# Kernel tuning notes

Measured on AMD Instinct MI355X. Metric: run time of the kernel, lower is better.

## Reference

```python
import jax, jax.numpy as jnp
import numpy as np

B, S, D = 2, 1024, 4096
N_HEADS, KV_HEADS, HEAD_DIM = 32, 8, 128
EPS = 1e-6
ROPE_THETA = 1e6


def setup_inputs() -> dict:
    key = jax.random.key(0)
    ks = jax.random.split(key, 7)
    scale = 0.02
    x = jax.random.normal(ks[0], (B, S, D), dtype=jnp.float32)
    positions = jnp.broadcast_to(jnp.arange(S, dtype=jnp.int32)[None, :], (B, S))
    wq = jax.random.normal(ks[1], (D, N_HEADS, HEAD_DIM), dtype=jnp.float32) * scale
    wk = jax.random.normal(ks[2], (D, KV_HEADS, HEAD_DIM), dtype=jnp.float32) * scale
    wv = jax.random.normal(ks[3], (D, KV_HEADS, HEAD_DIM), dtype=jnp.float32) * scale
    wo = jax.random.normal(ks[4], (N_HEADS, HEAD_DIM, D), dtype=jnp.float32) * scale
    q_norm_w = 1.0 + jax.random.normal(ks[5], (HEAD_DIM,), dtype=jnp.float32) * 0.01
    k_norm_w = 1.0 + jax.random.normal(ks[6], (HEAD_DIM,), dtype=jnp.float32) * 0.01
    return {"x": x, "positions": positions, "wq": wq, "wk": wk, "wv": wv,
            "wo": wo, "q_norm_w": q_norm_w, "k_norm_w": k_norm_w}


def _rms_norm(t, w):
    # per-head RMSNorm over last (head_dim) axis
    var = jnp.mean(jnp.square(t), axis=-1, keepdims=True)
    return (t * jax.lax.rsqrt(var + EPS)) * w


def _rope(t, positions):
    # neox-style rotary embedding; t: [B, S, n, H], positions: [B, S]
    half = t.shape[-1] // 2
    inv_freq = 1.0 / (ROPE_THETA ** (jnp.arange(0, half, dtype=jnp.float32) / half))
    ang = positions.astype(jnp.float32)[..., None] * inv_freq  # [B, S, half]
    cos = jnp.cos(ang)[:, :, None, :]  # [B, S, 1, half]
    sin = jnp.sin(ang)[:, :, None, :]
    t1, t2 = t[..., :half], t[..., half:]
    return jnp.concatenate([t1 * cos - t2 * sin, t2 * cos + t1 * sin], axis=-1)


def reference(x, positions, wq, wk, wv, wo, q_norm_w, k_norm_w):
    # QKV projections (einsum layers: 'bsd,dnh->bsnh')
    q = jnp.einsum('bsd,dnh->bsnh', x, wq)  # [B, S, N, H]
    k = jnp.einsum('bsd,dkh->bskh', x, wk)  # [B, S, K, H]
    v = jnp.einsum('bsd,dkh->bskh', x, wv)
    # per-head QK RMSNorm, then RoPE
    q = _rope(_rms_norm(q, q_norm_w), positions)
    k = _rope(_rms_norm(k, k_norm_w), positions)
    # GQA: expand KV heads to query heads
    groups = N_HEADS // KV_HEADS
    k = jnp.repeat(k, groups, axis=2)  # [B, S, N, H]
    v = jnp.repeat(v, groups, axis=2)
    sm_scale = HEAD_DIM ** -0.5
    scores = jnp.einsum('bqnh,btnh->bnqt', q, k) * sm_scale  # [B, N, S, S]
    causal = jnp.tril(jnp.ones((S, S), dtype=bool))
    scores = jnp.where(causal[None, None], scores, jnp.finfo(scores.dtype).min)
    probs = jax.nn.softmax(scores, axis=-1)
    attn = jnp.einsum('bnqt,btnh->bqnh', probs, v)  # [B, S, N, H]
    out = jnp.einsum('bqnh,nhd->bqd', attn, wo)  # output projection
    return out
```

## Files before the change

kernel.cpp:

```cpp
#include <hip/hip_runtime.h>
#include <stdint.h>

#define S_LEN   1024
#define D_MODEL 4096
#define NHQ     32
#define NKV     8
#define HD      128
#define NTOK    2048
#define NQKV    6144
#define SM_SCALE 0.08838834764831843f

typedef __attribute__((ext_vector_type(8))) __bf16 bf16x8;
typedef __attribute__((ext_vector_type(4))) float f32x4;

__device__ __forceinline__ unsigned short f2bf(float f) {
  union { float f; unsigned u; } x; x.f = f;
  unsigned r = x.u + 0x7fffu + ((x.u >> 16) & 1u);
  return (unsigned short)(r >> 16);
}

__device__ __forceinline__ void gload_lds16(const void* g, void* l) {
  __builtin_amdgcn_global_load_lds((__attribute__((address_space(1))) void*)g,
                                   (__attribute__((address_space(3))) void*)l,
                                   16, 0, 0);
}

__global__ void k_f32_to_bf16(const float* __restrict__ in,
                              unsigned short* __restrict__ out, int n8) {
  int i = blockIdx.x * blockDim.x + threadIdx.x;
  if (i >= n8) return;
  const float4* p = (const float4*)(in + (size_t)i * 8);
  float4 v0 = p[0], v1 = p[1];
  uint4 o;
  o.x = f2bf(v0.x) | ((unsigned)f2bf(v0.y) << 16);
  o.y = f2bf(v0.z) | ((unsigned)f2bf(v0.w) << 16);
  o.z = f2bf(v1.x) | ((unsigned)f2bf(v1.y) << 16);
  o.w = f2bf(v1.z) | ((unsigned)f2bf(v1.w) << 16);
  *(uint4*)(out + (size_t)i * 8) = o;
}

__global__ void k_transpose(const float* __restrict__ in,
                            unsigned short* __restrict__ out, int R, int C) {
  __shared__ float t[32][33];
  int c = threadIdx.x & 31, r0 = threadIdx.x >> 5;
  int cb = blockIdx.x * 32, rb = blockIdx.y * 32;
#pragma unroll
  for (int i = 0; i < 4; ++i) {
    int r = r0 + i * 8;
    t[r][c] = in[(size_t)(rb + r) * C + cb + c];
  }
  __syncthreads();
#pragma unroll
  for (int i = 0; i < 4; ++i) {
    int r = r0 + i * 8;
    out[(size_t)(cb + r) * R + rb + c] = f2bf(t[c][r]);
  }
}

__global__ __launch_bounds__(256) void k_gemm(
    const unsigned short* __restrict__ A,
    const unsigned short* __restrict__ Bt,
    float* __restrict__ C, int M, int N, int K, int ldc) {
  __shared__ __align__(16) unsigned short aT[128 * 32];
  __shared__ __align__(16) unsigned short bT[128 * 32];
  int tid = threadIdx.x;
  int w = tid >> 6, l = tid & 63;
  int lr = l & 15, lg = l >> 4;
  int bm = blockIdx.y * 128, bn = blockIdx.x * 128;
  int wr = (w >> 1) * 64, wc = (w & 1) * 64;
  f32x4 acc[4][4] = {};
  for (int k0 = 0; k0 < K; k0 += 32) {
    __syncthreads();
#pragma unroll
    for (int it = 0; it < 2; ++it) {
      int eo = (tid + it * 256) * 8;
      int r = eo >> 5, c = eo & 31;
      gload_lds16(A + (size_t)(bm + r) * K + k0 + c, (unsigned short*)aT + eo);
      gload_lds16(Bt + (size_t)(bn + r) * K + k0 + c, (unsigned short*)bT + eo);
    }
    __syncthreads();
    bf16x8 af[4], bfr[4];
#pragma unroll
    for (int r = 0; r < 4; ++r)
      af[r] = *(const bf16x8*)&aT[(wr + r * 16 + lr) * 32 + lg * 8];
#pragma unroll
    for (int c = 0; c < 4; ++c)
      bfr[c] = *(const bf16x8*)&bT[(wc + c * 16 + lr) * 32 + lg * 8];
#pragma unroll
    for (int r = 0; r < 4; ++r)
#pragma unroll
      for (int c = 0; c < 4; ++c)
        acc[r][c] = __builtin_amdgcn_mfma_f32_16x16x32_bf16(af[r], bfr[c], acc[r][c], 0, 0, 0);
  }
#pragma unroll
  for (int r = 0; r < 4; ++r)
#pragma unroll
    for (int c = 0; c < 4; ++c)
#pragma unroll
      for (int j = 0; j < 4; ++j)
        C[(size_t)(bm + wr + r * 16 + lg * 4 + j) * ldc + bn + wc + c * 16 + lr] = acc[r][c][j];
}

__global__ void k_norm_rope(const float* __restrict__ qkv, const float* __restrict__ w,
                            const int* __restrict__ positions,
                            unsigned short* __restrict__ out, int nheads, int colbase,
                            float oscale) {
  int wid = blockIdx.x * 4 + (threadIdx.x >> 6);
  int lane = threadIdx.x & 63;
  int token = wid / nheads, head = wid - token * nheads;
  const float* src = qkv + (size_t)token * NQKV + colbase + head * HD;
  float e0 = src[lane], e1 = src[lane + 64];
  float ss = e0 * e0 + e1 * e1;
#pragma unroll
  for (int m = 1; m < 64; m <<= 1) ss += __shfl_xor(ss, m, 64);
  float rs = rsqrtf(ss * (1.0f / 128.0f) + 1e-6f);
  float n0 = e0 * rs * w[lane], n1 = e1 * rs * w[lane + 64];
  int pos = positions[token];
  float invf = exp2f((float)lane * (-19.931568569324174f / 64.0f));
  float ang = (float)pos * invf;
  float sv, cv;
  sincosf(ang, &sv, &cv);
  float o0 = (n0 * cv - n1 * sv) * oscale;
  float o1 = (n1 * cv + n0 * sv) * oscale;
  int b = token >> 10, s = token & 1023;
  size_t ob = ((size_t)(b * nheads + head) * S_LEN + s) * HD;
  out[ob + lane] = f2bf(o0);
  out[ob + 64 + lane] = f2bf(o1);
}

__global__ void k_v_transpose(const float* __restrict__ qkv, unsigned short* __restrict__ vt) {
  __shared__ float t[32][33];
  int slice = blockIdx.z;
  int b = slice >> 3, kh = slice & 7;
  const float* in = qkv + (size_t)(b * S_LEN) * NQKV + 5120 + kh * HD;
  unsigned short* out = vt + (size_t)slice * HD * S_LEN;
  int c = threadIdx.x & 31, r0 = threadIdx.x >> 5;
  int s0 = blockIdx.y * 32, d0 = blockIdx.x * 32;
#pragma unroll
  for (int i = 0; i < 4; ++i) {
    int r = r0 + i * 8;
    t[r][c] = in[(size_t)(s0 + r) * NQKV + d0 + c];
  }
  __syncthreads();
#pragma unroll
  for (int i = 0; i < 4; ++i) {
    int r = r0 + i * 8;
    out[(size_t)(d0 + r) * S_LEN + s0 + c] = f2bf(t[c][r]);
  }
}

__global__ __launch_bounds__(256) void k_attn(const unsigned short* __restrict__ qh,
                                              const unsigned short* __restrict__ kbuf,
                                              const unsigned short* __restrict__ vtbuf,
                                              unsigned short* __restrict__ attn_out) {
  __shared__ __align__(16) unsigned short k_lds[64 * 128];
  __shared__ __align__(16) unsigned short v_lds[128 * 64];
  __shared__ __align__(16) unsigned short p_lds[4][16 * 64];
  int b = blockIdx.z, h = blockIdx.y, bx = blockIdx.x;
  int khd = h >> 2;
  int tid = threadIdx.x, w = tid >> 6, l = tid & 63;
  int lr = l & 15, lg = l >> 4;
  const unsigned short* K = kbuf + (size_t)(b * NKV + khd) * S_LEN * HD;
  const unsigned short* VT = vtbuf + (size_t)(b * NKV + khd) * HD * S_LEN;
  char* klp = (char*)k_lds;
  char* vlp = (char*)v_lds;
  char* plp = (char*)p_lds[w];
  int swz = (lr & 7) << 4;

  for (int strip = 0; strip < 2; ++strip) {
    int qs = strip ? (15 - bx) : bx;
    int q0 = qs * 64;
    const unsigned short* Q = qh + ((size_t)(b * NHQ + h) * S_LEN + q0 + w * 16) * HD;
    bf16x8 qf[4];
#pragma unroll
    for (int kk = 0; kk < 4; ++kk)
      qf[kk] = *(const bf16x8*)&Q[(size_t)lr * HD + kk * 32 + lg * 8];

    f32x4 o[8] = {};
    float m_[4], l_[4];
#pragma unroll
    for (int j = 0; j < 4; ++j) { m_[j] = -1e30f; l_[j] = 0.0f; }

    int nt = qs + 1;
    for (int t = 0; t < nt; ++t) {
      int t0 = t * 64;
      __syncthreads();
#pragma unroll
      for (int it = 0; it < 4; ++it) {
        int db = (tid + it * 256) * 16;
        int kr = db >> 8, kc = db & 255;
        gload_lds16(K + (size_t)(t0 + kr) * HD + ((kc ^ ((kr & 7) << 4)) >> 1), klp + db);
        int vr = db >> 7, vc = db & 127;
        gload_lds16(VT + (size_t)vr * S_LEN + t0 + ((vc ^ ((vr & 7) << 4)) >> 1), vlp + db);
      }
      __syncthreads();

      f32x4 sc[4];
      __builtin_amdgcn_s_setprio(1);
#pragma unroll
      for (int ct = 0; ct < 4; ++ct) {
        f32x4 s = {};
        int row = ct * 16 + lr;
#pragma unroll
        for (int kk = 0; kk < 4; ++kk) {
          bf16x8 kf = *(const bf16x8*)(klp + row * 256 + ((kk * 64 + lg * 16) ^ swz));
          s = __builtin_amdgcn_mfma_f32_16x16x32_bf16(qf[kk], kf, s, 0, 0, 0);
        }
        sc[ct] = s;
      }
      __builtin_amdgcn_s_setprio(0);

      bool full = (t < qs);
      float alpha[4];
#pragma unroll
      for (int j = 0; j < 4; ++j) {
        if (!full) {
          int rg = q0 + w * 16 + lg * 4 + j;
#pragma unroll
          for (int ct = 0; ct < 4; ++ct)
            sc[ct][j] = (t0 + ct * 16 + lr <= rg) ? sc[ct][j] : -1e30f;
        }
        float mx = fmaxf(fmaxf(sc[0][j], sc[1][j]), fmaxf(sc[2][j], sc[3][j]));
#pragma unroll
        for (int msk = 1; msk < 16; msk <<= 1) mx = fmaxf(mx, __shfl_xor(mx, msk, 64));
        float mn = fmaxf(m_[j], mx);
        alpha[j] = __expf(m_[j] - mn);
        int q = lg * 4 + j;
        int psw = (q & 7) << 4;
        float ps = 0.0f;
#pragma unroll
        for (int ct = 0; ct < 4; ++ct) {
          float p = __expf(sc[ct][j] - mn);
          ps += p;
          *(unsigned short*)(plp + q * 128 + (((ct * 16 + lr) * 2) ^ psw)) = f2bf(p);
        }
#pragma unroll
        for (int msk = 1; msk < 16; msk <<= 1) ps += __shfl_xor(ps, msk, 64);
        l_[j] = l_[j] * alpha[j] + ps;
        m_[j] = mn;
      }
#pragma unroll
      for (int dc = 0; dc < 8; ++dc) {
        o[dc][0] *= alpha[0]; o[dc][1] *= alpha[1];
        o[dc][2] *= alpha[2]; o[dc][3] *= alpha[3];
      }
      asm volatile("s_waitcnt lgkmcnt(0)" ::: "memory");
      __builtin_amdgcn_s_setprio(1);
#pragma unroll
      for (int kt = 0; kt < 2; ++kt) {
        bf16x8 pa = *(const bf16x8*)(plp + lr * 128 + ((kt * 64 + lg * 16) ^ swz));
#pragma unroll
        for (int dc = 0; dc < 8; ++dc) {
          int vrow = dc * 16 + lr;
          bf16x8 vf = *(const bf16x8*)(vlp + vrow * 128 + ((kt * 64 + lg * 16) ^ swz));
          o[dc] = __builtin_amdgcn_mfma_f32_16x16x32_bf16(pa, vf, o[dc], 0, 0, 0);
        }
      }
      __builtin_amdgcn_s_setprio(0);
    }

#pragma unroll
    for (int j = 0; j < 4; ++j) {
      int rg = q0 + w * 16 + lg * 4 + j;
      size_t row = (size_t)(b * S_LEN + rg) * D_MODEL + h * HD;
      float inv = 1.0f / l_[j];
#pragma unroll
      for (int dc = 0; dc < 8; ++dc)
        attn_out[row + dc * 16 + lr] = f2bf(o[dc][j] * inv);
    }
  }
}

extern "C" void kernel_launch(void* const* d_in, const int* in_sizes, int n_in,
                              void* d_out, int out_size, void* d_ws, size_t ws_size,
                              hipStream_t stream) {
  const float* x        = (const float*)d_in[0];
  const int* positions  = (const int*)d_in[1];
  const float* wq       = (const float*)d_in[2];
  const float* wk       = (const float*)d_in[3];
  const float* wv       = (const float*)d_in[4];
  const float* wo       = (const float*)d_in[5];
  const float* qnw      = (const float*)d_in[6];
  const float* knw      = (const float*)d_in[7];
  float* out            = (float*)d_out;

  char* ws = (char*)d_ws;
  unsigned short* xb   = (unsigned short*)(ws);
  unsigned short* wB   = (unsigned short*)(ws + 16777216);
  unsigned short* woT  = (unsigned short*)(ws + 67108864);
  float*          qkv  = (float*)(ws + 100663296);
  unsigned short* qh   = wB;
  unsigned short* khb  = (unsigned short*)(ws + 33554432);
  unsigned short* vtb  = (unsigned short*)(ws + 37748736);
  unsigned short* attn = xb;

  dim3 tb(256);
  k_f32_to_bf16<<<4096, tb, 0, stream>>>(x, xb, 1048576);
  k_transpose<<<dim3(128, 128), tb, 0, stream>>>(wq, wB, 4096, 4096);
  k_transpose<<<dim3(32, 128), tb, 0, stream>>>(wk, wB + (size_t)4096 * 4096, 4096, 1024);
  k_transpose<<<dim3(32, 128), tb, 0, stream>>>(wv, wB + (size_t)5120 * 4096, 4096, 1024);
  k_transpose<<<dim3(128, 128), tb, 0, stream>>>(wo, woT, 4096, 4096);

  k_gemm<<<dim3(48, 16), tb, 0, stream>>>(xb, wB, qkv, 2048, 6144, 4096, 6144);

  k_norm_rope<<<16384, tb, 0, stream>>>(qkv, qnw, positions, qh, 32, 0, SM_SCALE);
  k_norm_rope<<<4096, tb, 0, stream>>>(qkv, knw, positions, khb, 8, 4096, 1.0f);
  k_v_transpose<<<dim3(4, 32, 16), tb, 0, stream>>>(qkv, vtb);

  k_attn<<<dim3(8, 32, 2), tb, 0, stream>>>(qh, khb, vtb, attn);

  k_gemm<<<dim3(32, 16), tb, 0, stream>>>(attn, woT, out, 2048, 4096, 4096, 4096);
}
```

Baseline: 402.7 us.

## Replace 128x128 GEMM with double-buffered 256x256 tile pipelined MFMA kernel

Replaces the simple single-buffered 128x128 GEMM with a 256x256-tile, 512-thread kernel using 128KB of dynamic LDS. It double-buffers K=64 stages, issuing async global-to-LDS loads interleaved with MFMA phases, and XOR-swizzles LDS rows to avoid bank conflicts. It also remaps workgroup IDs across XCDs, raises priority during MFMA issue, and uses manual waitcnt/barrier scheduling. Both the QKV and output projections use it. The 256x256 tiles give only 192 and 128 workgroups, which underfills a 256-CU GPU, and the hand-tuned waitcnts risk subtle races.

```diff
diff --git a/kernel.cpp b/kernel.cpp
--- a/kernel.cpp
+++ b/kernel.cpp
@@ -57,48 +57,93 @@
   }
 }
 
-__global__ __launch_bounds__(256) void k_gemm(
+
+#define STG(Gptr, rowbase, ksrc, half, bufi, matoff)                            \
+  { int kcl = (ksrc) < NT ? (ksrc) : NT - 1;                                    \
+    _Pragma("unroll")                                                           \
+    for (int i_ = 0; i_ < 2; ++i_) {                                            \
+      int lin = i_ * 512 + tid;                                                 \
+      int r_ = lin >> 2, slot = lin & 3;                                        \
+      int sw = slot ^ ((r_ >> 1) & 3);                                          \
+      gload_lds16(Gptr + (size_t)((rowbase) + r_) * K + kcl * 64 + (half) * 32 + sw * 8, \
+                  smem + (bufi) * 65536 + (matoff) + (half) * 16384 + lin * 16); \
+    } }
+
+#define PHASE(mh, kstep, STAGE_STMT, DO_VMCNT)                                  \
+  {                                                                             \
+    const char* Ab = smem + cur * 65536 + (kstep) * 16384;                      \
+    const char* Bb = smem + cur * 65536 + 32768 + (kstep) * 16384;              \
+    bf16x8 af[4], bfr[4];                                                       \
+    _Pragma("unroll")                                                           \
+    for (int mf = 0; mf < 4; ++mf) {                                            \
+      int row = wr * 128 + (mh) * 64 + mf * 16 + lr;                            \
+      af[mf] = *(const bf16x8*)(Ab + row * 64 + ((lg * 16) ^ (((row >> 1) & 3) << 4))); \
+    }                                                                           \
+    _Pragma("unroll")                                                           \
+    for (int nf = 0; nf < 4; ++nf) {                                            \
+      int row = wc * 64 + nf * 16 + lr;                                         \
+      bfr[nf] = *(const bf16x8*)(Bb + row * 64 + ((lg * 16) ^ (((row >> 1) & 3) << 4))); \
+    }                                                                           \
+    STAGE_STMT;                                                                 \
+    if (DO_VMCNT) asm volatile("s_waitcnt vmcnt(6)" ::: "memory");              \
+    __builtin_amdgcn_s_barrier();                                               \
+    asm volatile("s_waitcnt lgkmcnt(0)" ::: "memory");                          \
+    __builtin_amdgcn_sched_barrier(0);                                          \
+    __builtin_amdgcn_s_setprio(1);                                              \
+    _Pragma("unroll")                                                           \
+    for (int mf = 0; mf < 4; ++mf)                                              \
+      _Pragma("unroll")                                                         \
+      for (int nf = 0; nf < 4; ++nf)                                            \
+        acc[(mh) * 4 + mf][nf] =                                                \
+            __builtin_amdgcn_mfma_f32_16x16x32_bf16(af[mf], bfr[nf], acc[(mh) * 4 + mf][nf], 0, 0, 0); \
+    __builtin_amdgcn_s_setprio(0);                                              \
+    __builtin_amdgcn_s_barrier();                                               \
+  }
+
+__global__ __launch_bounds__(512, 2) void k_gemm256(
     const unsigned short* __restrict__ A,
     const unsigned short* __restrict__ Bt,
-    float* __restrict__ C, int M, int N, int K, int ldc) {
-  __shared__ __align__(16) unsigned short aT[128 * 32];
-  __shared__ __align__(16) unsigned short bT[128 * 32];
+    float* __restrict__ C, int M, int N, int K, int ldc, int nbx) {
+  extern __shared__ __align__(16) char smem[];
   int tid = threadIdx.x;
-  int w = tid >> 6, l = tid & 63;
+  int l = tid & 63;
+  int w = tid >> 6;
   int lr = l & 15, lg = l >> 4;
-  int bm = blockIdx.y * 128, bn = blockIdx.x * 128;
-  int wr = (w >> 1) * 64, wc = (w & 1) * 64;
-  f32x4 acc[4][4] = {};
-  for (int k0 = 0; k0 < K; k0 += 32) {
-    __syncthreads();
-#pragma unroll
-    for (int it = 0; it < 2; ++it) {
-      int eo = (tid + it * 256) * 8;
-      int r = eo >> 5, c = eo & 31;
-      gload_lds16(A + (size_t)(bm + r) * K + k0 + c, (unsigned short*)aT + eo);
-      gload_lds16(Bt + (size_t)(bn + r) * K + k0 + c, (unsigned short*)bT + eo);
-    }
-    __syncthreads();
-    bf16x8 af[4], bfr[4];
-#pragma unroll
-    for (int r = 0; r < 4; ++r)
-      af[r] = *(const bf16x8*)&aT[(wr + r * 16 + lr) * 32 + lg * 8];
-#pragma unroll
-    for (int c = 0; c < 4; ++c)
-      bfr[c] = *(const bf16x8*)&bT[(wc + c * 16 + lr) * 32 + lg * 8];
-#pragma unroll
-    for (int r = 0; r < 4; ++r)
-#pragma unroll
-      for (int c = 0; c < 4; ++c)
-        acc[r][c] = __builtin_amdgcn_mfma_f32_16x16x32_bf16(af[r], bfr[c], acc[r][c], 0, 0, 0);
-  }
-#pragma unroll
-  for (int r = 0; r < 4; ++r)
-#pragma unroll
-    for (int c = 0; c < 4; ++c)
-#pragma unroll
-      for (int j = 0; j < 4; ++j)
-        C[(size_t)(bm + wr + r * 16 + lg * 4 + j) * ldc + bn + wc + c * 16 + lr] = acc[r][c][j];
+  int wr = w >> 2, wc = w & 3;
+  int nwg = gridDim.x;
+  int q8 = nwg >> 3;
+  int o = blockIdx.x;
+  int wg = (o & 7) * q8 + (o >> 3);
+  int by = wg / nbx, bx = wg - by * nbx;
+  int bm = by * 256, bn = bx * 256;
+  int NT = K >> 6;
+
+  f32x4 acc[8][4] = {};
+
+  STG(A, bm, 0, 0, 0, 0); STG(Bt, bn, 0, 0, 0, 32768);
+  STG(A, bm, 0, 1, 0, 0); STG(Bt, bn, 0, 1, 0, 32768);
+  STG(A, bm, 1, 0, 1, 0); STG(Bt, bn, 1, 0, 1, 32768);
+  asm volatile("s_waitcnt vmcnt(8)" ::: "memory");
+  __builtin_amdgcn_s_barrier();
+
+  for (int kt = 0; kt < NT; ++kt) {
+    int cur = kt & 1;
+    PHASE(0, 0, STG(A, bm, kt + 1, 1, cur ^ 1, 0), 0)
+    PHASE(1, 0, STG(Bt, bn, kt + 1, 1, cur ^ 1, 32768), 1)
+    PHASE(0, 1, STG(A, bm, kt + 2, 0, cur, 0), 0)
+    PHASE(1, 1, STG(Bt, bn, kt + 2, 0, cur, 32768), 1)
+  }
+
+#pragma unroll
+  for (int mh = 0; mh < 2; ++mh)
+#pragma unroll
+    for (int mf = 0; mf < 4; ++mf)
+#pragma unroll
+      for (int nf = 0; nf < 4; ++nf)
+#pragma unroll
+        for (int j = 0; j < 4; ++j)
+          C[(size_t)(bm + wr * 128 + mh * 64 + mf * 16 + lg * 4 + j) * ldc +
+            bn + wc * 64 + nf * 16 + lr] = acc[mh * 4 + mf][nf][j];
 }
 
 __global__ void k_norm_rope(const float* __restrict__ qkv, const float* __restrict__ w,
@@ -301,7 +346,7 @@
   k_transpose<<<dim3(32, 128), tb, 0, stream>>>(wv, wB + (size_t)5120 * 4096, 4096, 1024);
   k_transpose<<<dim3(128, 128), tb, 0, stream>>>(wo, woT, 4096, 4096);
 
-  k_gemm<<<dim3(48, 16), tb, 0, stream>>>(xb, wB, qkv, 2048, 6144, 4096, 6144);
+  k_gemm256<<<dim3(192), dim3(512), 131072, stream>>>(xb, wB, qkv, 2048, 6144, 4096, 6144, 24);
 
   k_norm_rope<<<16384, tb, 0, stream>>>(qkv, qnw, positions, qh, 32, 0, SM_SCALE);
   k_norm_rope<<<4096, tb, 0, stream>>>(qkv, knw, positions, khb, 8, 4096, 1.0f);
@@ -309,5 +354,5 @@
 
   k_attn<<<dim3(8, 32, 2), tb, 0, stream>>>(qh, khb, vtb, attn);
 
-  k_gemm<<<dim3(32, 16), tb, 0, stream>>>(attn, woT, out, 2048, 4096, 4096, 4096);
-}
+  k_gemm256<<<dim3(128), dim3(512), 131072, stream>>>(attn, woT, out, 2048, 4096, 4096, 4096, 16);
+}
```

Result: faster. 364.9 us (-9.4%).
